# Kernel optimization log

Hardware: AMD Instinct MI355X
Metric: run time of the kernel (lower is better)

Reference implementation:

```python
import jax, jax.numpy as jnp
import numpy as np

N_NODES = 50000
N_EDGES = 800000
IN_DIM = 64
HIDDEN = 64
N_LAYERS = 3
IMPROVED_FILL = 2.0  # improved_gcn=True -> self-loop weight 2
BN_EPS = 1e-5


def setup_inputs() -> dict:
    key = jax.random.key(0)
    ks = jax.random.split(key, 8)
    node_features = jax.random.normal(ks[0], (N_NODES, IN_DIM), dtype=jnp.float32)
    edge_indices = jax.random.randint(ks[1], (2, N_EDGES), 0, N_NODES, dtype=jnp.int64)
    edge_weight = jax.random.uniform(ks[2], (N_EDGES,), dtype=jnp.float32)
    # stacked per-layer params (in_dim == hidden_dim so weights stack cleanly)
    glorot = 1.0 / np.sqrt(HIDDEN)
    Ws = jax.random.uniform(ks[3], (N_LAYERS, HIDDEN, HIDDEN), minval=-glorot, maxval=glorot, dtype=jnp.float32)
    bs = jnp.zeros((N_LAYERS, HIDDEN), dtype=jnp.float32)
    gammas = jnp.ones((N_LAYERS, HIDDEN), dtype=jnp.float32)
    betas = jnp.zeros((N_LAYERS, HIDDEN), dtype=jnp.float32)
    return {"node_features": node_features, "edge_indices": edge_indices,
            "edge_weight": edge_weight, "Ws": Ws, "bs": bs,
            "gammas": gammas, "betas": betas}


def _gcn_layer(x, src, dst, w, W, b, gamma, beta):
    # GCNConv: x' = D^-1/2 (A + 2I) D^-1/2 (x W) + b  (improved=True)
    n = x.shape[0]
    lin = x @ W  # [N, H]
    loop_idx = jnp.arange(n, dtype=src.dtype)
    s = jnp.concatenate([src, loop_idx])
    d = jnp.concatenate([dst, loop_idx])
    wf = jnp.concatenate([w, jnp.full((n,), IMPROVED_FILL, dtype=w.dtype)])
    deg = jax.ops.segment_sum(wf, d, num_segments=n)
    dinv = jnp.where(deg > 0, jax.lax.rsqrt(deg), 0.0)
    norm = dinv[s] * wf * dinv[d]  # [E+N]
    agg = jax.ops.segment_sum(lin[s] * norm[:, None], d, num_segments=n)  # scatter-add
    h = jax.nn.relu(agg + b)
    # BatchNorm1d (training-mode batch stats, biased variance)
    mu = jnp.mean(h, axis=0)
    var = jnp.mean(jnp.square(h - mu), axis=0)
    h = (h - mu) * jax.lax.rsqrt(var + BN_EPS) * gamma + beta
    # Dropout treated as identity (eval / deterministic reference)
    return h


def reference(node_features, edge_indices, edge_weight, Ws, bs, gammas, betas):
    src, dst = edge_indices[0], edge_indices[1]
    h = node_features
    reps = []
    for i in range(N_LAYERS):
        h = _gcn_layer(h, src, dst, edge_weight, Ws[i], bs[i], gammas[i], betas[i])
        reps.append(h)
    return jnp.stack(reps)  # [n_layers, N, H] stacked intermediate reps
```

## Files before the change

kernel.cpp:

```cpp
#include <hip/hip_runtime.h>
#include <hip/hip_bf16.h>
#include <hip/hip_fp16.h>

#define N_NODES 50000
#define N_EDGES 800000
#define HID 64
#define N_LAYERS 3
#define BN_EPS 1e-5f
#define SELF_W 2.0f
#define BUCKET 48
#define NXCD 8
#define DSTRANGE 6250
#define GPB 1563
#define GN 196
#define GS 9375
#define GG 1563
#define GL 3125
#define NSTATS 16
#define Q18 262144.0f
#define Q18INV (1.0f / 262144.0f)

__device__ __forceinline__ unsigned short f2bf(float f) {
    return (unsigned short)((__float_as_uint(f) + 0x8000u) >> 16);
}
__device__ __forceinline__ float bf2f(unsigned short u) {
    return __uint_as_float(((unsigned)u) << 16);
}


__global__ void k_init(unsigned* __restrict__ packed4, float* __restrict__ statsP) {
    int i = blockIdx.x * blockDim.x + threadIdx.x;
    if (i < N_NODES) packed4[i] = 0u;
    if (i < N_LAYERS * NSTATS * 128) statsP[i] = 0.f;
}

__global__ void k_place(const int* __restrict__ src, const int* __restrict__ dst,
                        const float* __restrict__ w, unsigned* __restrict__ packed4,
                        unsigned* __restrict__ entries) {
    int group = blockIdx.x & (NXCD - 1);
    int big = blockIdx.x >> 3;
    int lo = group * DSTRANGE, hi = lo + DSTRANGE;
    int base = big * 512 + threadIdx.x;
#pragma unroll
    for (int r = 0; r < 2; ++r) {
        int e = base + r * 256;
        if (e < N_EDGES) {
            int d = dst[e];
            if (d >= lo && d < hi) {
                float wv = w[e];
                unsigned q = (unsigned)(wv * Q18 + 0.5f);
                unsigned old = atomicAdd(&packed4[d], (1u << 24) | q);
                int slot = (int)(old >> 24);
                unsigned hb = (unsigned)__half_as_ushort(__float2half(wv));
                entries[d * BUCKET + slot] = (hb << 16) | (unsigned)src[e];
            }
        }
    }
}

__global__ void k_norm_lin0(const unsigned* __restrict__ packed4,
                            unsigned* __restrict__ entries, float* __restrict__ selfnorm,
                            const float* __restrict__ x, const float* __restrict__ W0,
                            unsigned short* __restrict__ lin) {
    int tid = threadIdx.x;
    if (blockIdx.x < GS) {
        int idx = blockIdx.x * 256 + tid;
        int node = idx / BUCKET;
        int slot = idx - node * BUCKET;
        if (node < N_NODES) {
            unsigned pn = packed4[node];
            float din = rsqrtf(SELF_W + (float)(pn & 0xFFFFFFu) * Q18INV);
            if (slot == 0) selfnorm[node] = SELF_W * din * din;
            int cnt = (int)(pn >> 24);
            if (slot < cnt) {
                unsigned u = entries[idx];
                unsigned s = u & 0xFFFFu;
                float wv = __half2float(__ushort_as_half((unsigned short)(u >> 16)));
                unsigned ps = packed4[s];
                float dis = rsqrtf(SELF_W + (float)(ps & 0xFFFFFFu) * Q18INV);
                float n = wv * din * dis;
                entries[idx] = ((__float_as_uint(n) + 0x8000u) & 0xFFFF0000u) | s;
            }
        }
        return;
    }
    __shared__ float sW[HID * HID];
    __shared__ float sh[16][HID];
    for (int k = tid; k < HID * HID; k += 256) sW[k] = W0[k];
    int r = tid >> 6, c = tid & 63;
    int row0 = (blockIdx.x - GS) * 16;
#pragma unroll
    for (int i = 0; i < 4; ++i) {
        int row = row0 + r * 4 + i;
        sh[r * 4 + i][c] = x[(size_t)row * HID + c];
    }
    __syncthreads();
    float a0 = 0.f, a1 = 0.f, a2 = 0.f, a3 = 0.f;
#pragma unroll
    for (int k = 0; k < HID; ++k) {
        float wv = sW[k * HID + c];
        a0 = fmaf(sh[r * 4 + 0][k], wv, a0);
        a1 = fmaf(sh[r * 4 + 1][k], wv, a1);
        a2 = fmaf(sh[r * 4 + 2][k], wv, a2);
        a3 = fmaf(sh[r * 4 + 3][k], wv, a3);
    }
    lin[(size_t)(row0 + r * 4 + 0) * HID + c] = f2bf(a0);
    lin[(size_t)(row0 + r * 4 + 1) * HID + c] = f2bf(a1);
    lin[(size_t)(row0 + r * 4 + 2) * HID + c] = f2bf(a2);
    lin[(size_t)(row0 + r * 4 + 3) * HID + c] = f2bf(a3);
}


__global__ void k_gather(const unsigned short* __restrict__ lin,
                         const unsigned* __restrict__ entries,
                         const unsigned* __restrict__ packed4,
                         const float* __restrict__ selfnorm,
                         const float* __restrict__ b, unsigned short* __restrict__ hbuf,
                         float* __restrict__ statsP) {
    int tid = threadIdx.x;
    int wslot = __builtin_amdgcn_readfirstlane(tid >> 6);
    int nbase = blockIdx.x * 32 + wslot * 4;
    int lane = tid & 63;
    int g = lane >> 4;
    int quad = lane & 15;
    const ushort4* lin4 = (const ushort4*)lin;
    int n0 = nbase, n1 = nbase + 1, n2 = nbase + 2, n3 = nbase + 3;
    int c0 = (n0 < N_NODES) ? (int)(packed4[n0] >> 24) : 0;
    int c1 = (n1 < N_NODES) ? (int)(packed4[n1] >> 24) : 0;
    int c2 = (n2 < N_NODES) ? (int)(packed4[n2] >> 24) : 0;
    int c3 = (n3 < N_NODES) ? (int)(packed4[n3] >> 24) : 0;
    const unsigned* ep0 = entries + (size_t)(n0 < N_NODES ? n0 : 0) * BUCKET;
    const unsigned* ep1 = entries + (size_t)(n1 < N_NODES ? n1 : 0) * BUCKET;
    const unsigned* ep2 = entries + (size_t)(n2 < N_NODES ? n2 : 0) * BUCKET;
    const unsigned* ep3 = entries + (size_t)(n3 < N_NODES ? n3 : 0) * BUCKET;
    float a00 = 0.f, a01 = 0.f, a02 = 0.f, a03 = 0.f;
    float a10 = 0.f, a11 = 0.f, a12 = 0.f, a13 = 0.f;
    float a20 = 0.f, a21 = 0.f, a22 = 0.f, a23 = 0.f;
    float a30 = 0.f, a31 = 0.f, a32 = 0.f, a33 = 0.f;
    int cm01 = c0 > c1 ? c0 : c1;
    int cm23 = c2 > c3 ? c2 : c3;
    int cmax = cm01 > cm23 ? cm01 : cm23;
    for (int k = 0; k < cmax; k += 16) {
        unsigned e0[16], e1[16], e2[16], e3[16];
#pragma unroll
        for (int j = 0; j < 16; ++j) {
            e0[j] = ep0[k + j]; e1[j] = ep1[k + j];
            e2[j] = ep2[k + j]; e3[j] = ep3[k + j];
        }
#pragma unroll
        for (int j = 0; j < 4; ++j) {
            unsigned s0 = (g == 0) ? e0[j*4] : ((g == 1) ? e0[j*4+1] : ((g == 2) ? e0[j*4+2] : e0[j*4+3]));
            unsigned s1 = (g == 0) ? e1[j*4] : ((g == 1) ? e1[j*4+1] : ((g == 2) ? e1[j*4+2] : e1[j*4+3]));
            unsigned s2 = (g == 0) ? e2[j*4] : ((g == 1) ? e2[j*4+1] : ((g == 2) ? e2[j*4+2] : e2[j*4+3]));
            unsigned s3 = (g == 0) ? e3[j*4] : ((g == 1) ? e3[j*4+1] : ((g == 2) ? e3[j*4+2] : e3[j*4+3]));
            int kk = k + j * 4 + g;
            s0 = (kk < c0) ? s0 : 0u;
            s1 = (kk < c1) ? s1 : 0u;
            s2 = (kk < c2) ? s2 : 0u;
            s3 = (kk < c3) ? s3 : 0u;
            ushort4 u0 = lin4[(size_t)(s0 & 0xFFFFu) * 16 + quad];
            ushort4 u1 = lin4[(size_t)(s1 & 0xFFFFu) * 16 + quad];
            ushort4 u2 = lin4[(size_t)(s2 & 0xFFFFu) * 16 + quad];
            ushort4 u3 = lin4[(size_t)(s3 & 0xFFFFu) * 16 + quad];
            float nn0 = __uint_as_float(s0 & 0xFFFF0000u);
            float nn1 = __uint_as_float(s1 & 0xFFFF0000u);
            float nn2 = __uint_as_float(s2 & 0xFFFF0000u);
            float nn3 = __uint_as_float(s3 & 0xFFFF0000u);
            a00 = fmaf(bf2f(u0.x), nn0, a00); a01 = fmaf(bf2f(u0.y), nn0, a01);
            a02 = fmaf(bf2f(u0.z), nn0, a02); a03 = fmaf(bf2f(u0.w), nn0, a03);
            a10 = fmaf(bf2f(u1.x), nn1, a10); a11 = fmaf(bf2f(u1.y), nn1, a11);
            a12 = fmaf(bf2f(u1.z), nn1, a12); a13 = fmaf(bf2f(u1.w), nn1, a13);
            a20 = fmaf(bf2f(u2.x), nn2, a20); a21 = fmaf(bf2f(u2.y), nn2, a21);
            a22 = fmaf(bf2f(u2.z), nn2, a22); a23 = fmaf(bf2f(u2.w), nn2, a23);
            a30 = fmaf(bf2f(u3.x), nn3, a30); a31 = fmaf(bf2f(u3.y), nn3, a31);
            a32 = fmaf(bf2f(u3.z), nn3, a32); a33 = fmaf(bf2f(u3.w), nn3, a33);
        }
    }
    a00 += __shfl_xor(a00, 16); a01 += __shfl_xor(a01, 16);
    a02 += __shfl_xor(a02, 16); a03 += __shfl_xor(a03, 16);
    a10 += __shfl_xor(a10, 16); a11 += __shfl_xor(a11, 16);
    a12 += __shfl_xor(a12, 16); a13 += __shfl_xor(a13, 16);
    a20 += __shfl_xor(a20, 16); a21 += __shfl_xor(a21, 16);
    a22 += __shfl_xor(a22, 16); a23 += __shfl_xor(a23, 16);
    a30 += __shfl_xor(a30, 16); a31 += __shfl_xor(a31, 16);
    a32 += __shfl_xor(a32, 16); a33 += __shfl_xor(a33, 16);
    a00 += __shfl_xor(a00, 32); a01 += __shfl_xor(a01, 32);
    a02 += __shfl_xor(a02, 32); a03 += __shfl_xor(a03, 32);
    a10 += __shfl_xor(a10, 32); a11 += __shfl_xor(a11, 32);
    a12 += __shfl_xor(a12, 32); a13 += __shfl_xor(a13, 32);
    a20 += __shfl_xor(a20, 32); a21 += __shfl_xor(a21, 32);
    a22 += __shfl_xor(a22, 32); a23 += __shfl_xor(a23, 32);
    a30 += __shfl_xor(a30, 32); a31 += __shfl_xor(a31, 32);
    a32 += __shfl_xor(a32, 32); a33 += __shfl_xor(a33, 32);
    __shared__ float ls[32][HID], ls2[32][HID];
    int node = (g == 0) ? n0 : ((g == 1) ? n1 : ((g == 2) ? n2 : n3));
    float b0 = (g == 0) ? a00 : ((g == 1) ? a10 : ((g == 2) ? a20 : a30));
    float b1 = (g == 0) ? a01 : ((g == 1) ? a11 : ((g == 2) ? a21 : a31));
    float b2 = (g == 0) ? a02 : ((g == 1) ? a12 : ((g == 2) ? a22 : a32));
    float b3 = (g == 0) ? a03 : ((g == 1) ? a13 : ((g == 2) ? a23 : a33));
    int rr = wslot * 4 + g;
    int cb = quad * 4;
    float tx = 0.f, ty = 0.f, tz = 0.f, tw = 0.f;
    if (node < N_NODES) {
        ushort4 u = lin4[(size_t)node * 16 + quad];
        float sn = selfnorm[node];
        float4 b4 = ((const float4*)b)[quad];
        tx = fmaf(bf2f(u.x), sn, b0) + b4.x;
        ty = fmaf(bf2f(u.y), sn, b1) + b4.y;
        tz = fmaf(bf2f(u.z), sn, b2) + b4.z;
        tw = fmaf(bf2f(u.w), sn, b3) + b4.w;
        tx = tx > 0.f ? tx : 0.f;
        ty = ty > 0.f ? ty : 0.f;
        tz = tz > 0.f ? tz : 0.f;
        tw = tw > 0.f ? tw : 0.f;
        ushort4 h4;
        h4.x = f2bf(tx); h4.y = f2bf(ty); h4.z = f2bf(tz); h4.w = f2bf(tw);
        ((ushort4*)hbuf)[(size_t)node * 16 + quad] = h4;
    }
    ls[rr][cb + 0] = tx; ls[rr][cb + 1] = ty;
    ls[rr][cb + 2] = tz; ls[rr][cb + 3] = tw;
    ls2[rr][cb + 0] = tx * tx; ls2[rr][cb + 1] = ty * ty;
    ls2[rr][cb + 2] = tz * tz; ls2[rr][cb + 3] = tw * tw;
    __syncthreads();
    float* sp = statsP + (size_t)(blockIdx.x & (NSTATS - 1)) * 128;
    if (tid < HID) {
        float s = 0.f;
#pragma unroll
        for (int rv = 0; rv < 32; ++rv) s += ls[rv][tid];
        atomicAdd(&sp[tid], s);
    } else if (tid < 2 * HID) {
        int cc = tid - HID;
        float s = 0.f;
#pragma unroll
        for (int rv = 0; rv < 32; ++rv) s += ls2[rv][cc];
        atomicAdd(&sp[HID + cc], s);
    }
}

__global__ void k_bnlin(const unsigned short* __restrict__ hbuf,
                        const float* __restrict__ statsP,
                        const float* __restrict__ gamma, const float* __restrict__ beta,
                        const float* __restrict__ W, float* __restrict__ out,
                        unsigned short* __restrict__ lin) {
    __shared__ float sW[HID * HID];
    __shared__ float sh[16][HID];
    __shared__ float s_sc[HID], s_sf[HID];
    int tid = threadIdx.x;
    for (int k = tid; k < HID * HID; k += 256) sW[k] = W[k];
    if (tid < HID) {
        float s = 0.f, s2 = 0.f;
#pragma unroll
        for (int i = 0; i < NSTATS; ++i) {
            s  += statsP[i * 128 + tid];
            s2 += statsP[i * 128 + HID + tid];
        }
        const float invn = 1.0f / (float)N_NODES;
        float mu = s * invn;
        float var = s2 * invn - mu * mu;
        float sc = rsqrtf(var + BN_EPS) * gamma[tid];
        s_sc[tid] = sc;
        s_sf[tid] = beta[tid] - mu * sc;
    }
    __syncthreads();
    int r = tid >> 6, c = tid & 63;
    float sc = s_sc[c], sf = s_sf[c];
    int row0 = blockIdx.x * 16;
#pragma unroll
    for (int i = 0; i < 4; ++i) {
        int row = row0 + r * 4 + i;
        float val = bf2f(hbuf[(size_t)row * HID + c]) * sc + sf;
        __builtin_nontemporal_store(val, &out[(size_t)row * HID + c]);
        sh[r * 4 + i][c] = val;
    }
    __syncthreads();
    float a0 = 0.f, a1 = 0.f, a2 = 0.f, a3 = 0.f;
#pragma unroll
    for (int k = 0; k < HID; ++k) {
        float wv = sW[k * HID + c];
        a0 = fmaf(sh[r * 4 + 0][k], wv, a0);
        a1 = fmaf(sh[r * 4 + 1][k], wv, a1);
        a2 = fmaf(sh[r * 4 + 2][k], wv, a2);
        a3 = fmaf(sh[r * 4 + 3][k], wv, a3);
    }
    lin[(size_t)(row0 + r * 4 + 0) * HID + c] = f2bf(a0);
    lin[(size_t)(row0 + r * 4 + 1) * HID + c] = f2bf(a1);
    lin[(size_t)(row0 + r * 4 + 2) * HID + c] = f2bf(a2);
    lin[(size_t)(row0 + r * 4 + 3) * HID + c] = f2bf(a3);
}

__global__ void k_bn_apply(const unsigned short* __restrict__ hbuf,
                           const float* __restrict__ statsP,
                           const float* __restrict__ gamma, const float* __restrict__ beta,
                           float* __restrict__ out) {
    __shared__ float s_sc[HID], s_sf[HID];
    int tid = threadIdx.x;
    if (tid < HID) {
        float s = 0.f, s2 = 0.f;
#pragma unroll
        for (int i = 0; i < NSTATS; ++i) {
            s  += statsP[i * 128 + tid];
            s2 += statsP[i * 128 + HID + tid];
        }
        const float invn = 1.0f / (float)N_NODES;
        float mu = s * invn;
        float var = s2 * invn - mu * mu;
        float sc = rsqrtf(var + BN_EPS) * gamma[tid];
        s_sc[tid] = sc;
        s_sf[tid] = beta[tid] - mu * sc;
    }
    __syncthreads();
    int r = tid >> 6, c = tid & 63;
    float sc = s_sc[c], sf = s_sf[c];
    int row0 = blockIdx.x * 16;
#pragma unroll
    for (int i = 0; i < 4; ++i) {
        int row = row0 + r * 4 + i;
        float val = bf2f(hbuf[(size_t)row * HID + c]) * sc + sf;
        __builtin_nontemporal_store(val, &out[(size_t)row * HID + c]);
    }
}


extern "C" void kernel_launch(void* const* d_in, const int* in_sizes, int n_in,
                              void* d_out, int out_size, void* d_ws, size_t ws_size,
                              hipStream_t stream) {
    const float* x      = (const float*)d_in[0];
    const int*   ei     = (const int*)d_in[1];
    const float* w      = (const float*)d_in[2];
    const float* Ws     = (const float*)d_in[3];
    const float* bs     = (const float*)d_in[4];
    const float* gammas = (const float*)d_in[5];
    const float* betas  = (const float*)d_in[6];
    float* out = (float*)d_out;

    const int* src = ei;
    const int* dst = ei + N_EDGES;

    unsigned* packed4 = (unsigned*)d_ws;
    unsigned* entries = packed4 + N_NODES;
    float*  selfnorm = (float*)(entries + (size_t)N_NODES * BUCKET);
    float*  statsP   = selfnorm + N_NODES;
    unsigned short* lin  = (unsigned short*)(statsP + N_LAYERS * NSTATS * 128);
    unsigned short* hbuf = lin + (size_t)N_NODES * HID;

    const int T = 256;

    k_init<<<GN, T, 0, stream>>>(packed4, statsP);
    k_place<<<NXCD * GPB, T, 0, stream>>>(src, dst, w, packed4, entries);
    k_norm_lin0<<<GS + GL, T, 0, stream>>>(packed4, entries, selfnorm, x, Ws, lin);

    for (int L = 0; L < N_LAYERS; ++L) {
        float* outL = out + (size_t)L * N_NODES * HID;
        const float* b  = bs + (size_t)L * HID;
        const float* g  = gammas + (size_t)L * HID;
        const float* bt = betas + (size_t)L * HID;
        float* statsL = statsP + (size_t)L * NSTATS * 128;

        k_gather<<<GG, 512, 0, stream>>>(lin, entries, packed4, selfnorm, b, hbuf, statsL);
        if (L < N_LAYERS - 1) {
            const float* Wn = Ws + (size_t)(L + 1) * HID * HID;
            k_bnlin<<<GL, T, 0, stream>>>(hbuf, statsL, g, bt, Wn, outL, lin);
        } else {
            k_bn_apply<<<GL, T, 0, stream>>>(hbuf, statsL, g, bt, outL);
        }
    }
}
```

Measured before the change: 177.9 us.

## Sort gather nodes by degree class to balance per-wave edge loops

Adds a kernel that buckets nodes into classes by ceil(degree/16) and writes a permutation, so the gather kernel processes groups of four nodes with similar degree. Because each wave loops to the maximum degree of its four nodes, this is meant to cut the wasted iterations caused by mixing low- and high-degree nodes. In exchange it adds one launch in which every block scans all node degrees, plus an extra indirection in the gather. Node writes become scattered rather than contiguous, which may hurt locality for the hbuf stores and the BN statistics.

```diff
diff --git a/kernel.cpp b/kernel.cpp
--- a/kernel.cpp
+++ b/kernel.cpp
@@ -28,10 +28,12 @@
 }
 
 
-__global__ void k_init(unsigned* __restrict__ packed4, float* __restrict__ statsP) {
+__global__ void k_init(unsigned* __restrict__ packed4, float* __restrict__ statsP,
+                       unsigned* __restrict__ clsCursor) {
     int i = blockIdx.x * blockDim.x + threadIdx.x;
     if (i < N_NODES) packed4[i] = 0u;
     if (i < N_LAYERS * NSTATS * 128) statsP[i] = 0.f;
+    if (i < 4) clsCursor[i] = 0u;
 }
 
 __global__ void k_place(const int* __restrict__ src, const int* __restrict__ dst,
@@ -110,29 +112,69 @@
     lin[(size_t)(row0 + r * 4 + 3) * HID + c] = f2bf(a3);
 }
 
+__global__ void k_perm(const unsigned* __restrict__ packed4,
+                       unsigned* __restrict__ clsCursor, int* __restrict__ perm) {
+    int tid = threadIdx.x;
+    unsigned h0 = 0, h1 = 0, h2 = 0, h3 = 0;
+    for (int i = tid; i < N_NODES; i += 256) {
+        int cls = ((int)(packed4[i] >> 24) + 15) >> 4;
+        h0 += (cls == 0); h1 += (cls == 1); h2 += (cls == 2); h3 += (cls == 3);
+    }
+#pragma unroll
+    for (int off = 32; off; off >>= 1) {
+        h0 += __shfl_down(h0, off); h1 += __shfl_down(h1, off);
+        h2 += __shfl_down(h2, off); h3 += __shfl_down(h3, off);
+    }
+    __shared__ unsigned hs[4][4];
+    int wv = tid >> 6, ln = tid & 63;
+    if (ln == 0) { hs[wv][0] = h0; hs[wv][1] = h1; hs[wv][2] = h2; hs[wv][3] = h3; }
+    __syncthreads();
+    __shared__ unsigned start[4], lcnt[4], lbase[4];
+    if (tid < 4) {
+        unsigned s = 0;
+        for (int c = 0; c < tid; ++c) s += hs[0][c] + hs[1][c] + hs[2][c] + hs[3][c];
+        start[tid] = s;
+        lcnt[tid] = 0;
+    }
+    __syncthreads();
+    int node = blockIdx.x * 256 + tid;
+    int cls = 0; unsigned lrank = 0;
+    if (node < N_NODES) {
+        cls = ((int)(packed4[node] >> 24) + 15) >> 4;
+        lrank = atomicAdd(&lcnt[cls], 1u);
+    }
+    __syncthreads();
+    if (tid < 4) lbase[tid] = atomicAdd(&clsCursor[tid], lcnt[tid]);
+    __syncthreads();
+    if (node < N_NODES) perm[start[cls] + lbase[cls] + lrank] = node;
+}
+
 
 __global__ void k_gather(const unsigned short* __restrict__ lin,
                          const unsigned* __restrict__ entries,
                          const unsigned* __restrict__ packed4,
                          const float* __restrict__ selfnorm,
-                         const float* __restrict__ b, unsigned short* __restrict__ hbuf,
-                         float* __restrict__ statsP) {
+                         const float* __restrict__ b, const int* __restrict__ perm,
+                         unsigned short* __restrict__ hbuf, float* __restrict__ statsP) {
     int tid = threadIdx.x;
     int wslot = __builtin_amdgcn_readfirstlane(tid >> 6);
-    int nbase = blockIdx.x * 32 + wslot * 4;
+    int idx0 = blockIdx.x * 32 + wslot * 4;
     int lane = tid & 63;
     int g = lane >> 4;
     int quad = lane & 15;
     const ushort4* lin4 = (const ushort4*)lin;
-    int n0 = nbase, n1 = nbase + 1, n2 = nbase + 2, n3 = nbase + 3;
-    int c0 = (n0 < N_NODES) ? (int)(packed4[n0] >> 24) : 0;
-    int c1 = (n1 < N_NODES) ? (int)(packed4[n1] >> 24) : 0;
-    int c2 = (n2 < N_NODES) ? (int)(packed4[n2] >> 24) : 0;
-    int c3 = (n3 < N_NODES) ? (int)(packed4[n3] >> 24) : 0;
-    const unsigned* ep0 = entries + (size_t)(n0 < N_NODES ? n0 : 0) * BUCKET;
-    const unsigned* ep1 = entries + (size_t)(n1 < N_NODES ? n1 : 0) * BUCKET;
-    const unsigned* ep2 = entries + (size_t)(n2 < N_NODES ? n2 : 0) * BUCKET;
-    const unsigned* ep3 = entries + (size_t)(n3 < N_NODES ? n3 : 0) * BUCKET;
+    int n0 = (idx0 + 0 < N_NODES) ? perm[idx0 + 0] : -1;
+    int n1 = (idx0 + 1 < N_NODES) ? perm[idx0 + 1] : -1;
+    int n2 = (idx0 + 2 < N_NODES) ? perm[idx0 + 2] : -1;
+    int n3 = (idx0 + 3 < N_NODES) ? perm[idx0 + 3] : -1;
+    int c0 = (n0 >= 0) ? (int)(packed4[n0] >> 24) : 0;
+    int c1 = (n1 >= 0) ? (int)(packed4[n1] >> 24) : 0;
+    int c2 = (n2 >= 0) ? (int)(packed4[n2] >> 24) : 0;
+    int c3 = (n3 >= 0) ? (int)(packed4[n3] >> 24) : 0;
+    const unsigned* ep0 = entries + (size_t)(n0 >= 0 ? n0 : 0) * BUCKET;
+    const unsigned* ep1 = entries + (size_t)(n1 >= 0 ? n1 : 0) * BUCKET;
+    const unsigned* ep2 = entries + (size_t)(n2 >= 0 ? n2 : 0) * BUCKET;
+    const unsigned* ep3 = entries + (size_t)(n3 >= 0 ? n3 : 0) * BUCKET;
     float a00 = 0.f, a01 = 0.f, a02 = 0.f, a03 = 0.f;
     float a10 = 0.f, a11 = 0.f, a12 = 0.f, a13 = 0.f;
     float a20 = 0.f, a21 = 0.f, a22 = 0.f, a23 = 0.f;
@@ -201,7 +243,7 @@
     int rr = wslot * 4 + g;
     int cb = quad * 4;
     float tx = 0.f, ty = 0.f, tz = 0.f, tw = 0.f;
-    if (node < N_NODES) {
+    if (node >= 0) {
         ushort4 u = lin4[(size_t)node * 16 + quad];
         float sn = selfnorm[node];
         float4 b4 = ((const float4*)b)[quad];
@@ -340,14 +382,17 @@
     unsigned* entries = packed4 + N_NODES;
     float*  selfnorm = (float*)(entries + (size_t)N_NODES * BUCKET);
     float*  statsP   = selfnorm + N_NODES;
-    unsigned short* lin  = (unsigned short*)(statsP + N_LAYERS * NSTATS * 128);
+    unsigned* clsCursor = (unsigned*)(statsP + N_LAYERS * NSTATS * 128);
+    int*    perm     = (int*)(clsCursor + 8);
+    unsigned short* lin  = (unsigned short*)(perm + N_NODES);
     unsigned short* hbuf = lin + (size_t)N_NODES * HID;
 
     const int T = 256;
 
-    k_init<<<GN, T, 0, stream>>>(packed4, statsP);
+    k_init<<<GN, T, 0, stream>>>(packed4, statsP, clsCursor);
     k_place<<<NXCD * GPB, T, 0, stream>>>(src, dst, w, packed4, entries);
     k_norm_lin0<<<GS + GL, T, 0, stream>>>(packed4, entries, selfnorm, x, Ws, lin);
+    k_perm<<<GN, T, 0, stream>>>(packed4, clsCursor, perm);
 
     for (int L = 0; L < N_LAYERS; ++L) {
         float* outL = out + (size_t)L * N_NODES * HID;
@@ -356,7 +401,7 @@
         const float* bt = betas + (size_t)L * HID;
         float* statsL = statsP + (size_t)L * NSTATS * 128;
 
-        k_gather<<<GG, 512, 0, stream>>>(lin, entries, packed4, selfnorm, b, hbuf, statsL);
+        k_gather<<<GG, 512, 0, stream>>>(lin, entries, packed4, selfnorm, b, perm, hbuf, statsL);
         if (L < N_LAYERS - 1) {
             const float* Wn = Ws + (size_t)(L + 1) * HID * HID;
             k_bnlin<<<GL, T, 0, stream>>>(hbuf, statsL, g, bt, Wn, outL, lin);
```

After: 205.6 us. 15.6% more time.
